# Performance work log

Measured on AMD Instinct MI355X. Metric: run time of the kernel, lower is better.

Reference implementation:

```python
import math
import jax
import jax.numpy as jnp
import numpy as np

B, T, D = 1, 2048, 1024
H, KV, DH = 16, 4, 64
E, TOPK, DFF = 32, 4, 1024
WINDOW = 128
EPS = 1e-5
ROPE_BASE = 150000.0
ROPE_SCALE = 32.0


def setup_inputs() -> dict:
    key = jax.random.key(0)
    ks = jax.random.split(key, 12)
    s = 0.02  # init scale for stability
    return {
        "x": jax.random.normal(ks[0], (B, T, D), jnp.float32),
        "attn_norm_w": 1.0 + 0.02 * jax.random.normal(ks[1], (D,), jnp.float32),
        "ffn_norm_w": 1.0 + 0.02 * jax.random.normal(ks[2], (D,), jnp.float32),
        "qkv_w": s * jax.random.normal(ks[3], (D, H * DH + 2 * KV * DH), jnp.float32),
        "qkv_b": s * jax.random.normal(ks[4], (H * DH + 2 * KV * DH,), jnp.float32),
        "proj_w": s * jax.random.normal(ks[5], (H * DH, D), jnp.float32),
        "proj_b": s * jax.random.normal(ks[6], (D,), jnp.float32),
        "attn_sink": 0.5 * jax.random.normal(ks[7], (H,), jnp.float32),
        "gate_w": s * jax.random.normal(ks[8], (D, E), jnp.float32),
        "gate_b": s * jax.random.normal(ks[9], (E,), jnp.float32),
        "W_up": s * jax.random.normal(ks[10], (E, D, 2 * DFF), jnp.float32),
        "W_down": s * jax.random.normal(ks[11], (E, DFF, D), jnp.float32),
    }


def _rmsnorm(x, w):
    rms = jax.lax.rsqrt(jnp.mean(x * x, axis=-1, keepdims=True) + EPS)
    return w * (x * rms)


def _apply_rope(x, sin, cos):
    # x: [B, h, T, dh]; sin/cos: [T, dh//2] -> interleaved rotation
    x1, x2 = x[..., ::2], x[..., 1::2]
    out = jnp.stack([x1 * cos - x2 * sin, x1 * sin + x2 * cos], axis=-1)
    return out.reshape(x.shape)


def reference(x, attn_norm_w, ffn_norm_w, qkv_w, qkv_b, proj_w, proj_b,
              attn_sink, gate_w, gate_b, W_up, W_down):
    Bx, Tx, Dx = x.shape
    # ---- attention branch ----
    h = _rmsnorm(x, attn_norm_w)
    qkv = h @ qkv_w + qkv_b
    q = qkv[..., : H * DH].reshape(Bx, Tx, H, DH).transpose(0, 2, 1, 3)
    k = qkv[..., H * DH : H * DH + KV * DH].reshape(Bx, Tx, KV, DH).transpose(0, 2, 1, 3)
    v = qkv[..., H * DH + KV * DH :].reshape(Bx, Tx, KV, DH).transpose(0, 2, 1, 3)
    # RoPE angles: pos/scale * base^{-2i/dh}
    pos = jnp.arange(Tx, dtype=jnp.float32) / ROPE_SCALE
    inv_freq = 1.0 / (ROPE_BASE ** (jnp.arange(0, DH, 2, dtype=jnp.float32) / DH))
    freqs = pos[:, None] * inv_freq[None, :]  # [T, DH//2]
    sin, cos = jnp.sin(freqs), jnp.cos(freqs)
    q = _apply_rope(q, sin, cos)
    k = _apply_rope(k, sin, cos)
    rep = H // KV
    k = jnp.repeat(k, rep, axis=1)
    v = jnp.repeat(v, rep, axis=1)
    logits = jnp.einsum('bhqd,bhkd->bhqk', q, k) / math.sqrt(DH)
    i = jnp.arange(Tx)[:, None]
    j = jnp.arange(Tx)[None, :]
    mask = (j > i) | (i - j > WINDOW)  # sliding-window causal
    logits = jnp.where(mask, -jnp.inf, logits)
    lse = jax.nn.logsumexp(logits, axis=-1, keepdims=True)  # [B,H,T,1]
    denom_log = jnp.logaddexp(lse, attn_sink.reshape(1, H, 1, 1))
    attn = jnp.exp(logits - denom_log)  # rows sum to < 1 due to sink
    y = jnp.einsum('bhqk,bhkd->bhqd', attn, v)
    y = y.transpose(0, 2, 1, 3).reshape(Bx, Tx, H * DH)
    x = x + (y @ proj_w + proj_b)
    # ---- token-choice MoE branch ----
    h2 = _rmsnorm(x, ffn_norm_w).reshape(Bx * Tx, Dx)
    glogits = h2 @ gate_w + gate_b  # [N, E]
    topv, topi = jax.lax.top_k(glogits, TOPK)
    gw = jax.nn.softmax(topv, axis=-1)  # [N, TOPK]
    N = Bx * Tx
    combine = jnp.zeros((N, E), x.dtype).at[jnp.arange(N)[:, None], topi].add(gw)
    def body(acc, we):
        wu, wd, ce = we  # [D,2DFF], [DFF,D], [N]
        ug = h2 @ wu
        u, g = ug[:, :DFF], ug[:, DFF:]
        return acc + ce[:, None] * ((jax.nn.silu(g) * u) @ wd), None
    y2, _ = jax.lax.scan(body, jnp.zeros_like(h2), (W_up, W_down, combine.T))
    return x + y2.reshape(Bx, Tx, Dx)
```

## Files before the change

### kernel.cpp

```cpp
#include <hip/hip_runtime.h>
#include <hip/hip_bf16.h>

#define NEx 32
#define QKVN 1536
#define MAXTILES 96

typedef __attribute__((ext_vector_type(4))) float f32x4_t;
typedef __attribute__((ext_vector_type(8))) __bf16 bf16x8_t;

__device__ __forceinline__ unsigned short f2bfu(float f) {
  union { float f; unsigned int u; } a; a.f = f;
  unsigned int r = a.u + 0x7fffu + ((a.u >> 16) & 1u);
  return (unsigned short)(r >> 16);
}
__device__ __forceinline__ float bf2f(unsigned short u) {
  union { unsigned int u; float f; } a; a.u = ((unsigned int)u) << 16; return a.f;
}
__device__ __forceinline__ uint2 pack4u(unsigned short a, unsigned short b,
                                        unsigned short c, unsigned short d) {
  return make_uint2((unsigned int)a | ((unsigned int)b << 16),
                    (unsigned int)c | ((unsigned int)d << 16));
}
__device__ __forceinline__ void split2(float v, unsigned short& hi, unsigned short& lo) {
  hi = f2bfu(v);
  lo = f2bfu(v - bf2f(hi));
}
typedef const __attribute__((address_space(1))) void* gas_t;
typedef __attribute__((address_space(3))) void* las_t;
__device__ __forceinline__ void gl16(const void* g, void* l) {
  __builtin_amdgcn_global_load_lds((gas_t)g, (las_t)l, 16, 0, 0);
}

template<int SPLIT>
__global__ __launch_bounds__(256) void k_wT(const float* __restrict__ in,
    unsigned short* __restrict__ outh, unsigned short* __restrict__ outl, int N) {
  __shared__ float T[64][68];
  int k0 = blockIdx.x * 64, n0 = blockIdx.y * 64, e = blockIdx.z;
  const float* src = in + (size_t)e * 1024 * N;
  int t = threadIdx.x;
  int rk = t >> 2, c4 = (t & 3) * 4;
#pragma unroll
  for (int j = 0; j < 4; ++j) {
    int col = c4 + j * 16;
    f32x4_t v = *(const f32x4_t*)(src + (size_t)(k0 + rk) * N + n0 + col);
    *(f32x4_t*)&T[rk][col] = v;
  }
  __syncthreads();
  int nn = t >> 2, kc0 = (t & 3) * 16;
  size_t orow = ((size_t)e * N + n0 + nn) * 1024 + k0;
#pragma unroll
  for (int j = 0; j < 2; ++j) {
    int kc = kc0 + j * 8;
    unsigned short hi[8], lo[8];
#pragma unroll
    for (int q = 0; q < 8; ++q) split2(T[kc + q][nn], hi[q], lo[q]);
    uint2 a = pack4u(hi[0], hi[1], hi[2], hi[3]);
    uint2 b = pack4u(hi[4], hi[5], hi[6], hi[7]);
    *(uint4*)(outh + orow + kc) = make_uint4(a.x, a.y, b.x, b.y);
    if (SPLIT) {
      uint2 c = pack4u(lo[0], lo[1], lo[2], lo[3]);
      uint2 d = pack4u(lo[4], lo[5], lo[6], lo[7]);
      *(uint4*)(outl + orow + kc) = make_uint4(c.x, c.y, d.x, d.y);
    }
  }
}

__global__ __launch_bounds__(256) void k_rmsnorm_s(const float* __restrict__ x,
    const float* __restrict__ w, unsigned short* __restrict__ ph, unsigned short* __restrict__ pl) {
  int row = blockIdx.x, tid = threadIdx.x;
  f32x4_t v = *(const f32x4_t*)(x + (size_t)row * 1024 + tid * 4);
  float ss = v.x * v.x + v.y * v.y + v.z * v.z + v.w * v.w;
#pragma unroll
  for (int o = 32; o > 0; o >>= 1) ss += __shfl_xor(ss, o);
  __shared__ float red[4];
  if ((tid & 63) == 0) red[tid >> 6] = ss;
  __syncthreads();
  float sc = rsqrtf((red[0] + red[1] + red[2] + red[3]) * (1.f / 1024.f) + 1e-5f);
  const float* wr = w + tid * 4;
  ushort4 h4, l4;
  split2(v.x * sc * wr[0], h4.x, l4.x);
  split2(v.y * sc * wr[1], h4.y, l4.y);
  split2(v.z * sc * wr[2], h4.z, l4.z);
  split2(v.w * sc * wr[3], h4.w, l4.w);
  *(ushort4*)(ph + (size_t)row * 1024 + tid * 4) = h4;
  *(ushort4*)(pl + (size_t)row * 1024 + tid * 4) = l4;
}

__global__ __launch_bounds__(256) void k_rmsnorm_f(const float* __restrict__ x,
    const float* __restrict__ w, float* __restrict__ outf, unsigned short* __restrict__ outb,
    float* __restrict__ y2) {
  int row = blockIdx.x, tid = threadIdx.x;
  f32x4_t v = *(const f32x4_t*)(x + (size_t)row * 1024 + tid * 4);
  *(f32x4_t*)(y2 + (size_t)row * 1024 + tid * 4) = (f32x4_t){0.f, 0.f, 0.f, 0.f};
  float ss = v.x * v.x + v.y * v.y + v.z * v.z + v.w * v.w;
#pragma unroll
  for (int o = 32; o > 0; o >>= 1) ss += __shfl_xor(ss, o);
  __shared__ float red[4];
  if ((tid & 63) == 0) red[tid >> 6] = ss;
  __syncthreads();
  float sc = rsqrtf((red[0] + red[1] + red[2] + red[3]) * (1.f / 1024.f) + 1e-5f);
  const float* wr = w + tid * 4;
  f32x4_t o4;
  o4.x = v.x * sc * wr[0]; o4.y = v.y * sc * wr[1];
  o4.z = v.z * sc * wr[2]; o4.w = v.w * sc * wr[3];
  *(f32x4_t*)(outf + (size_t)row * 1024 + tid * 4) = o4;
  ushort4 b4;
  b4.x = f2bfu(o4.x); b4.y = f2bfu(o4.y); b4.z = f2bfu(o4.z); b4.w = f2bfu(o4.w);
  *(ushort4*)(outb + (size_t)row * 1024 + tid * 4) = b4;
}

template<int RES>
__global__ __launch_bounds__(256) void k_gemm_s(
    const unsigned short* __restrict__ Ahg, const unsigned short* __restrict__ Alg,
    const unsigned short* __restrict__ BhT, const unsigned short* __restrict__ BlT,
    const float* __restrict__ bias, const float* __restrict__ res,
    float* __restrict__ C, int N) {
  __shared__ unsigned short Ah[64 * 32], Al[64 * 32], Bh[128 * 32], Bl[128 * 32];
  int tid = threadIdx.x, lane = tid & 63, w = tid >> 6;
  int m0 = blockIdx.y * 64, n0 = blockIdx.x * 128;
  int wm = (w >> 1) * 32, wn = (w & 1) * 64;
  int rl = lane >> 2, koff = (lane & 3) * 8;
  const unsigned short* agh = Ahg + (size_t)(m0 + w * 16 + rl) * 1024 + koff;
  const unsigned short* agl = Alg + (size_t)(m0 + w * 16 + rl) * 1024 + koff;
  const unsigned short* bgh0 = BhT + (size_t)(n0 + (w * 2 + 0) * 16 + rl) * 1024 + koff;
  const unsigned short* bgh1 = BhT + (size_t)(n0 + (w * 2 + 1) * 16 + rl) * 1024 + koff;
  const unsigned short* bgl0 = BlT + (size_t)(n0 + (w * 2 + 0) * 16 + rl) * 1024 + koff;
  const unsigned short* bgl1 = BlT + (size_t)(n0 + (w * 2 + 1) * 16 + rl) * 1024 + koff;
  f32x4_t acc[2][4];
#pragma unroll
  for (int i = 0; i < 2; ++i)
#pragma unroll
    for (int j = 0; j < 4; ++j) acc[i][j] = (f32x4_t){0.f, 0.f, 0.f, 0.f};
  int fr = lane & 15, fc = (lane >> 4) * 8;
  for (int k0 = 0; k0 < 1024; k0 += 32) {
    gl16(agh + k0, (char*)Ah + w * 1024);
    gl16(agl + k0, (char*)Al + w * 1024);
    gl16(bgh0 + k0, (char*)Bh + (w * 2 + 0) * 1024);
    gl16(bgh1 + k0, (char*)Bh + (w * 2 + 1) * 1024);
    gl16(bgl0 + k0, (char*)Bl + (w * 2 + 0) * 1024);
    gl16(bgl1 + k0, (char*)Bl + (w * 2 + 1) * 1024);
    __syncthreads();
    bf16x8_t fah[2], fal[2], fbh[4], fbl[4];
#pragma unroll
    for (int mi = 0; mi < 2; ++mi) {
      fah[mi] = *(const bf16x8_t*)(Ah + (wm + mi * 16 + fr) * 32 + fc);
      fal[mi] = *(const bf16x8_t*)(Al + (wm + mi * 16 + fr) * 32 + fc);
    }
#pragma unroll
    for (int nj = 0; nj < 4; ++nj) {
      fbh[nj] = *(const bf16x8_t*)(Bh + (wn + nj * 16 + fr) * 32 + fc);
      fbl[nj] = *(const bf16x8_t*)(Bl + (wn + nj * 16 + fr) * 32 + fc);
    }
#pragma unroll
    for (int mi = 0; mi < 2; ++mi)
#pragma unroll
      for (int nj = 0; nj < 4; ++nj) {
        acc[mi][nj] = __builtin_amdgcn_mfma_f32_16x16x32_bf16(fah[mi], fbh[nj], acc[mi][nj], 0, 0, 0);
        acc[mi][nj] = __builtin_amdgcn_mfma_f32_16x16x32_bf16(fah[mi], fbl[nj], acc[mi][nj], 0, 0, 0);
        acc[mi][nj] = __builtin_amdgcn_mfma_f32_16x16x32_bf16(fal[mi], fbh[nj], acc[mi][nj], 0, 0, 0);
      }
    __syncthreads();
  }
  int frow = (lane >> 4) * 4;
#pragma unroll
  for (int mi = 0; mi < 2; ++mi)
#pragma unroll
    for (int nj = 0; nj < 4; ++nj) {
      int col = n0 + wn + nj * 16 + fr;
      float bv = bias[col];
#pragma unroll
      for (int r = 0; r < 4; ++r) {
        int row = m0 + wm + mi * 16 + frow + r;
        float v = acc[mi][nj][r] + bv;
        if (RES) v += res[(size_t)row * N + col];
        C[(size_t)row * N + col] = v;
      }
    }
}

__global__ __launch_bounds__(256) void k_rope(float* __restrict__ qkv) {
  int idx = blockIdx.x * 256 + threadIdx.x;
  int i = idx & 31;
  int r5 = idx >> 5;
  int hd = r5 % 20, t = r5 / 20;
  int col = (hd < 16) ? hd * 64 : 1024 + (hd - 16) * 64;
  float* p = qkv + (size_t)t * QKVN + col + 2 * i;
  float2 v = *(float2*)p;
  float invf = exp2f(-(float)i * (17.194602975157967f / 32.f));
  float ang = ((float)t * (1.f / 32.f)) * invf;
  float s, c;
  sincosf(ang, &s, &c);
  float2 o; o.x = v.x * c - v.y * s; o.y = v.x * s + v.y * c;
  *(float2*)p = o;
}

__global__ __launch_bounds__(256) void k_attn(const float* __restrict__ qkv,
    const float* __restrict__ sink, unsigned short* __restrict__ yh,
    unsigned short* __restrict__ yl) {
  __shared__ float Kl[72 * 65];
  __shared__ float Vl[72 * 64];
  __shared__ float ql[16][64];
  __shared__ float pl[4][128];
  int i0 = blockIdx.x * 16, hh = blockIdx.y;
  int g = hh >> 2;
  int jb = i0 - 128; if (jb < 0) jb = 0;
  int nk = i0 + 16 - jb;
  int tid = threadIdx.x, wid = tid >> 6, lane = tid & 63;
  {
    int r = tid >> 4, d4 = (tid & 15) * 4;
    *(f32x4_t*)&ql[r][d4] = *(const f32x4_t*)(qkv + (size_t)(i0 + r) * QKVN + hh * 64 + d4);
  }
  float sk = sink[hh];
  float m_[4], s_[4], y_[4];
#pragma unroll
  for (int qq = 0; qq < 4; ++qq) { m_[qq] = sk; s_[qq] = 0.f; y_[qq] = 0.f; }
  int nch = (nk + 71) / 72;
  int cbase = 0;
  for (int ch = 0; ch < nch; ++ch) {
    int csz = nk - cbase; if (csz > 72) csz = 72;
    __syncthreads();
    for (int id = tid; id < csz * 16; id += 256) {
      int c = id >> 4, d4 = (id & 15) * 4;
      const float* kp = qkv + (size_t)(jb + cbase + c) * QKVN + 1024 + g * 64 + d4;
      *(f32x4_t*)&Kl[c * 65 + d4] = *(const f32x4_t*)kp;
      *(f32x4_t*)&Vl[c * 64 + d4] = *(const f32x4_t*)(kp + 256);
    }
    __syncthreads();
#pragma unroll
    for (int qq = 0; qq < 4; ++qq) {
      int qr = wid * 4 + qq;
      int cm = i0 + qr - jb;
      int s1 = lane + 64;
      int r1 = (s1 < csz) ? s1 : (csz - 1);
      const float* k0p = Kl + lane * 65;
      const float* k1p = Kl + r1 * 65;
      float a0 = 0.f, a1 = 0.f;
#pragma unroll 4
      for (int d = 0; d < 64; ++d) {
        float qd = ql[qr][d];
        a0 += qd * k0p[d];
        a1 += qd * k1p[d];
      }
      int c0 = cbase + lane, c1 = cbase + s1;
      bool ok0 = (lane < csz) && (c0 <= cm) && (c0 >= cm - 128);
      bool ok1 = (s1 < csz) && (c1 <= cm) && (c1 >= cm - 128);
      float l0 = ok0 ? a0 * 0.125f : -1e30f;
      float l1 = ok1 ? a1 * 0.125f : -1e30f;
      float mc = fmaxf(l0, l1);
#pragma unroll
      for (int o = 32; o > 0; o >>= 1) mc = fmaxf(mc, __shfl_xor(mc, o));
      float mo = m_[qq];
      float mn = fmaxf(mo, mc);
      float fac = __expf(mo - mn);
      float p0 = __expf(l0 - mn), p1 = __expf(l1 - mn);
      float ps = p0 + p1;
#pragma unroll
      for (int o = 32; o > 0; o >>= 1) ps += __shfl_xor(ps, o);
      m_[qq] = mn;
      s_[qq] = s_[qq] * fac + ps;
      pl[wid][lane] = p0;
      pl[wid][s1] = p1;
      __syncthreads();
      float y = y_[qq] * fac;
      for (int s = 0; s < csz; ++s) y += pl[wid][s] * Vl[s * 64 + lane];
      y_[qq] = y;
      __syncthreads();
    }
    cbase += csz;
  }
#pragma unroll
  for (int qq = 0; qq < 4; ++qq) {
    float inv = 1.f / (s_[qq] + __expf(sk - m_[qq]));
    int i = i0 + wid * 4 + qq;
    unsigned short hi, lo;
    split2(y_[qq] * inv, hi, lo);
    yh[(size_t)i * 1024 + hh * 64 + lane] = hi;
    yl[(size_t)i * 1024 + hh * 64 + lane] = lo;
  }
}

__global__ __launch_bounds__(64) void k_gate(const float* __restrict__ h2f,
    const float* __restrict__ gw, const float* __restrict__ gb,
    int* __restrict__ texp, float* __restrict__ twt) {
  int t = blockIdx.x, l = threadIdx.x;
  int e = l & 31, half = l >> 5;
  const float* hr = h2f + (size_t)t * 1024 + half * 512;
  const float* wp = gw + (size_t)half * 512 * 32 + e;
  float s = 0;
  for (int d = 0; d < 512; ++d) s += hr[d] * wp[(size_t)d * 32];
  s += __shfl_xor(s, 32);
  __shared__ float gl[32];
  if (l < 32) gl[l] = s + gb[e];
  __syncthreads();
  if (l == 0) {
    int bi[4]; float bv[4];
    for (int j = 0; j < 4; ++j) {
      int mi_ = 0; float mv = gl[0];
      for (int q = 1; q < 32; ++q) if (gl[q] > mv) { mv = gl[q]; mi_ = q; }
      bi[j] = mi_; bv[j] = mv; gl[mi_] = -1e30f;
    }
    float mx = bv[0], sum = 0, wv[4];
    for (int j = 0; j < 4; ++j) { wv[j] = __expf(bv[j] - mx); sum += wv[j]; }
    float inv = 1.f / sum;
    for (int j = 0; j < 4; ++j) { texp[t * 4 + j] = bi[j]; twt[t * 4 + j] = wv[j] * inv; }
  }
}

__global__ __launch_bounds__(256) void k_moe_count(const int* __restrict__ texp, int* __restrict__ cnt) {
  int e = blockIdx.x, tid = threadIdx.x;
  int c = 0;
  for (int i = tid; i < 8192; i += 256) c += (texp[i] == e);
#pragma unroll
  for (int o = 32; o > 0; o >>= 1) c += __shfl_xor(c, o);
  __shared__ int red[4];
  if ((tid & 63) == 0) red[tid >> 6] = c;
  __syncthreads();
  if (tid == 0) cnt[e] = red[0] + red[1] + red[2] + red[3];
}

__global__ void k_moe_off(const int* __restrict__ cnt, int* __restrict__ off,
                          int* __restrict__ tiles) {
  if (threadIdx.x == 0) {
    int s = 0, t = 0;
    for (int e = 0; e < NEx; ++e) {
      off[e] = s;
      int nt = (cnt[e] + 127) >> 7;
      for (int j = 0; j < nt; ++j) tiles[t++] = e | (j << 8);
      s += cnt[e];
    }
    for (; t < MAXTILES; ++t) tiles[t] = -1;
  }
}

__global__ __launch_bounds__(256) void k_moe_assign(const int* __restrict__ texp,
    const float* __restrict__ twt, const int* __restrict__ off,
    int* __restrict__ slot_token, float* __restrict__ slot_wt) {
  int e = blockIdx.x, tid = threadIdx.x;
  int b0 = tid * 32;
  int c = 0;
  for (int i = 0; i < 32; ++i) c += (texp[b0 + i] == e);
  __shared__ int pre[256];
  pre[tid] = c;
  __syncthreads();
  for (int d = 1; d < 256; d <<= 1) {
    int v = (tid >= d) ? pre[tid - d] : 0;
    __syncthreads();
    pre[tid] += v;
    __syncthreads();
  }
  int run = off[e] + pre[tid] - c;
  for (int i = 0; i < 32; ++i) {
    int idx = b0 + i;
    if (texp[idx] == e) {
      slot_token[run] = idx >> 2;
      slot_wt[run] = twt[idx];
      ++run;
    }
  }
}

__global__ __launch_bounds__(256) void k_moe_up(const unsigned short* __restrict__ h2b,
    const unsigned short* __restrict__ WupT, const int* __restrict__ cnt,
    const int* __restrict__ off, const int* __restrict__ tiles,
    const int* __restrict__ slot_token, unsigned short* __restrict__ act) {
  int code = tiles[blockIdx.y];
  if (code < 0) return;
  int e = code & 255;
  int m0 = (code >> 8) << 7;
  int ne = cnt[e];
  int n0 = blockIdx.x * 64;
  int base = off[e];
  __shared__ unsigned short Asm[128 * 32];
  __shared__ unsigned short Bsm[128 * 32];
  int tid = threadIdx.x, lane = tid & 63, w = tid >> 6;
  int rl = lane >> 2, koff = (lane & 3) * 8;
  const unsigned short* ag[2];
  const unsigned short* bg[2];
#pragma unroll
  for (int i = 0; i < 2; ++i) {
    int row = (w * 2 + i) * 16 + rl;
    int tok = (m0 + row < ne) ? slot_token[base + m0 + row] : 0;
    ag[i] = h2b + (size_t)tok * 1024 + koff;
    int grow = (row < 64) ? (n0 + row) : (1024 + n0 + row - 64);
    bg[i] = WupT + (size_t)e * 2048 * 1024 + (size_t)grow * 1024 + koff;
  }
  f32x4_t acc[2][8];
#pragma unroll
  for (int i = 0; i < 2; ++i)
#pragma unroll
    for (int j = 0; j < 8; ++j) acc[i][j] = (f32x4_t){0.f, 0.f, 0.f, 0.f};
  int fr = lane & 15, fc = (lane >> 4) * 8;
  for (int k0 = 0; k0 < 1024; k0 += 32) {
    gl16(ag[0] + k0, (char*)Asm + (w * 2 + 0) * 1024);
    gl16(ag[1] + k0, (char*)Asm + (w * 2 + 1) * 1024);
    gl16(bg[0] + k0, (char*)Bsm + (w * 2 + 0) * 1024);
    gl16(bg[1] + k0, (char*)Bsm + (w * 2 + 1) * 1024);
    __syncthreads();
    bf16x8_t af[2], bfr[8];
#pragma unroll
    for (int mi = 0; mi < 2; ++mi)
      af[mi] = *(const bf16x8_t*)(Asm + (w * 32 + mi * 16 + fr) * 32 + fc);
#pragma unroll
    for (int nj = 0; nj < 8; ++nj)
      bfr[nj] = *(const bf16x8_t*)(Bsm + (nj * 16 + fr) * 32 + fc);
#pragma unroll
    for (int mi = 0; mi < 2; ++mi)
#pragma unroll
      for (int nj = 0; nj < 8; ++nj)
        acc[mi][nj] = __builtin_amdgcn_mfma_f32_16x16x32_bf16(af[mi], bfr[nj], acc[mi][nj], 0, 0, 0);
    __syncthreads();
  }
  int frow = (lane >> 4) * 4;
#pragma unroll
  for (int mi = 0; mi < 2; ++mi)
#pragma unroll
    for (int r = 0; r < 4; ++r) {
      int row = m0 + w * 32 + mi * 16 + frow + r;
      if (row < ne) {
#pragma unroll
        for (int nj = 0; nj < 4; ++nj) {
          float u = acc[mi][nj][r];
          float gg = acc[mi][nj + 4][r];
          float sig = 1.f / (1.f + __expf(-gg));
          act[(size_t)(base + row) * 1024 + n0 + nj * 16 + fr] = f2bfu(u * gg * sig);
        }
      }
    }
}

__global__ __launch_bounds__(256) void k_moe_down(const unsigned short* __restrict__ act,
    const unsigned short* __restrict__ WdnT, const int* __restrict__ cnt,
    const int* __restrict__ off, const int* __restrict__ tiles,
    const int* __restrict__ slot_token, const float* __restrict__ slot_wt,
    float* __restrict__ y2) {
  int code = tiles[blockIdx.y];
  if (code < 0) return;
  int e = code & 255;
  int m0 = (code >> 8) << 7;
  int ne = cnt[e];
  int n0 = blockIdx.x * 128;
  int base = off[e];
  __shared__ unsigned short Asm[128 * 32];
  __shared__ unsigned short Bsm[128 * 32];
  int tid = threadIdx.x, lane = tid & 63, w = tid >> 6;
  int wm = (w >> 1) * 64, wn = (w & 1) * 64;
  int rl = lane >> 2, koff = (lane & 3) * 8;
  const unsigned short* ag[2];
  const unsigned short* bg[2];
#pragma unroll
  for (int i = 0; i < 2; ++i) {
    int row = (w * 2 + i) * 16 + rl;
    ag[i] = act + (size_t)(base + m0 + row) * 1024 + koff;
    bg[i] = WdnT + (size_t)e * 1024 * 1024 + (size_t)(n0 + row) * 1024 + koff;
  }
  f32x4_t acc[4][4];
#pragma unroll
  for (int i = 0; i < 4; ++i)
#pragma unroll
    for (int j = 0; j < 4; ++j) acc[i][j] = (f32x4_t){0.f, 0.f, 0.f, 0.f};
  int fr = lane & 15, fc = (lane >> 4) * 8;
  for (int k0 = 0; k0 < 1024; k0 += 32) {
    gl16(ag[0] + k0, (char*)Asm + (w * 2 + 0) * 1024);
    gl16(ag[1] + k0, (char*)Asm + (w * 2 + 1) * 1024);
    gl16(bg[0] + k0, (char*)Bsm + (w * 2 + 0) * 1024);
    gl16(bg[1] + k0, (char*)Bsm + (w * 2 + 1) * 1024);
    __syncthreads();
    bf16x8_t af[4], bfr[4];
#pragma unroll
    for (int mi = 0; mi < 4; ++mi)
      af[mi] = *(const bf16x8_t*)(Asm + (wm + mi * 16 + fr) * 32 + fc);
#pragma unroll
    for (int nj = 0; nj < 4; ++nj)
      bfr[nj] = *(const bf16x8_t*)(Bsm + (wn + nj * 16 + fr) * 32 + fc);
#pragma unroll
    for (int mi = 0; mi < 4; ++mi)
#pragma unroll
      for (int nj = 0; nj < 4; ++nj)
        acc[mi][nj] = __builtin_amdgcn_mfma_f32_16x16x32_bf16(af[mi], bfr[nj], acc[mi][nj], 0, 0, 0);
    __syncthreads();
  }
  int frow = (lane >> 4) * 4;
#pragma unroll
  for (int mi = 0; mi < 4; ++mi)
#pragma unroll
    for (int r = 0; r < 4; ++r) {
      int row = m0 + wm + mi * 16 + frow + r;
      if (row < ne) {
        int slot = base + row;
        int token = slot_token[slot];
        float wt = slot_wt[slot];
#pragma unroll
        for (int nj = 0; nj < 4; ++nj) {
          int col = n0 + wn + nj * 16 + fr;
          atomicAdd(&y2[(size_t)token * 1024 + col], wt * acc[mi][nj][r]);
        }
      }
    }
}

__global__ __launch_bounds__(256) void k_final(const float* __restrict__ x1,
    const float* __restrict__ y2, float* __restrict__ out) {
  int idx = blockIdx.x * 256 + threadIdx.x;
  f32x4_t a = *(const f32x4_t*)(x1 + (size_t)idx * 4);
  f32x4_t b = *(const f32x4_t*)(y2 + (size_t)idx * 4);
  a = a + b;
  *(f32x4_t*)(out + (size_t)idx * 4) = a;
}

extern "C" void kernel_launch(void* const* d_in, const int* in_sizes, int n_in,
                              void* d_out, int out_size, void* d_ws, size_t ws_size,
                              hipStream_t stream) {
  const float* x           = (const float*)d_in[0];
  const float* attn_norm_w = (const float*)d_in[1];
  const float* ffn_norm_w  = (const float*)d_in[2];
  const float* qkv_w       = (const float*)d_in[3];
  const float* qkv_b       = (const float*)d_in[4];
  const float* proj_w      = (const float*)d_in[5];
  const float* proj_b      = (const float*)d_in[6];
  const float* attn_sink   = (const float*)d_in[7];
  const float* gate_w      = (const float*)d_in[8];
  const float* gate_b      = (const float*)d_in[9];
  const float* W_up        = (const float*)d_in[10];
  const float* W_down      = (const float*)d_in[11];
  float* out = (float*)d_out;

  char* ws = (char*)d_ws;
  size_t o = 0;
  auto alloc = [&](size_t bytes) -> void* {
    void* p = ws + o;
    o = (o + bytes + 255) & ~(size_t)255;
    return p;
  };
  unsigned short* WT      = (unsigned short*)alloc((size_t)32 * 2048 * 1024 * 2);
  unsigned short* qkvThi  = (unsigned short*)alloc((size_t)1536 * 1024 * 2);
  unsigned short* qkvTlo  = (unsigned short*)alloc((size_t)1536 * 1024 * 2);
  unsigned short* projThi = (unsigned short*)alloc((size_t)1024 * 1024 * 2);
  unsigned short* projTlo = (unsigned short*)alloc((size_t)1024 * 1024 * 2);
  unsigned short* pAhi    = (unsigned short*)alloc((size_t)2048 * 1024 * 2);
  unsigned short* pAlo    = (unsigned short*)alloc((size_t)2048 * 1024 * 2);
  float* qkv              = (float*)alloc((size_t)2048 * 1536 * 4);
  float* x1               = (float*)alloc((size_t)2048 * 1024 * 4);
  unsigned short* act     = (unsigned short*)alloc((size_t)(8192 + 128) * 1024 * 2);
  float* y2               = (float*)alloc((size_t)2048 * 1024 * 4);
  int* texp               = (int*)alloc(8192 * 4);
  float* twt              = (float*)alloc(8192 * 4);
  int* cnt                = (int*)alloc(256);
  int* offs               = (int*)alloc(256);
  int* tiles              = (int*)alloc(MAXTILES * 4);
  int* slot_token         = (int*)alloc(8192 * 4);
  float* slot_wt          = (float*)alloc(8192 * 4);
  float* h2f              = qkv;
  unsigned short* h2b     = (unsigned short*)(qkv + (size_t)2048 * 1024);

  k_wT<1><<<dim3(16, 24, 1), 256, 0, stream>>>(qkv_w, qkvThi, qkvTlo, 1536);
  k_wT<1><<<dim3(16, 16, 1), 256, 0, stream>>>(proj_w, projThi, projTlo, 1024);
  k_wT<0><<<dim3(16, 32, 32), 256, 0, stream>>>(W_up, WT, nullptr, 2048);

  k_rmsnorm_s<<<2048, 256, 0, stream>>>(x, attn_norm_w, pAhi, pAlo);
  k_gemm_s<0><<<dim3(12, 32), 256, 0, stream>>>(pAhi, pAlo, qkvThi, qkvTlo, qkv_b, nullptr, qkv, 1536);
  k_rope<<<5120, 256, 0, stream>>>(qkv);
  k_attn<<<dim3(128, 16), 256, 0, stream>>>(qkv, attn_sink, pAhi, pAlo);
  k_gemm_s<1><<<dim3(8, 32), 256, 0, stream>>>(pAhi, pAlo, projThi, projTlo, proj_b, x, x1, 1024);
  k_rmsnorm_f<<<2048, 256, 0, stream>>>(x1, ffn_norm_w, h2f, h2b, y2);
  k_gate<<<2048, 64, 0, stream>>>(h2f, gate_w, gate_b, texp, twt);
  k_moe_count<<<32, 256, 0, stream>>>(texp, cnt);
  k_moe_off<<<1, 64, 0, stream>>>(cnt, offs, tiles);
  k_moe_assign<<<32, 256, 0, stream>>>(texp, twt, offs, slot_token, slot_wt);
  k_moe_up<<<dim3(16, MAXTILES), 256, 0, stream>>>(h2b, WT, cnt, offs, tiles, slot_token, act);
  k_wT<0><<<dim3(16, 16, 32), 256, 0, stream>>>(W_down, WT, nullptr, 1024);
  k_moe_down<<<dim3(8, MAXTILES), 256, 0, stream>>>(act, WT, cnt, offs, tiles, slot_token, slot_wt, y2);
  k_final<<<2048, 256, 0, stream>>>(x1, y2, out);
}
```

Before: 475.9 us.

## Fuse gate into FFN RMSNorm and double-buffer LDS in GEMM kernels

The router gate matmul and top-k selection now run inside the FFN RMSNorm kernel, so the fp32 normalized activations no longer go to global memory and no separate gate launch is needed. All three MFMA GEMM kernels (split-precision projection, MoE up, MoE down) now use two LDS buffers and prefetch the next K tile while the current one is computed. The per-iteration barrier count drops from two to one. The cost is double the shared memory, which may lower occupancy, and 32 accumulator registers plus a long shuffle reduction per thread in the fused norm kernel.

```diff
diff --git a/kernel.cpp b/kernel.cpp
--- a/kernel.cpp
+++ b/kernel.cpp
@@ -86,9 +86,10 @@
   *(ushort4*)(pl + (size_t)row * 1024 + tid * 4) = l4;
 }
 
-__global__ __launch_bounds__(256) void k_rmsnorm_f(const float* __restrict__ x,
-    const float* __restrict__ w, float* __restrict__ outf, unsigned short* __restrict__ outb,
-    float* __restrict__ y2) {
+__global__ __launch_bounds__(256) void k_rmsnorm_g(const float* __restrict__ x,
+    const float* __restrict__ w, const float* __restrict__ gw, const float* __restrict__ gb,
+    unsigned short* __restrict__ outb, float* __restrict__ y2,
+    int* __restrict__ texp, float* __restrict__ twt) {
   int row = blockIdx.x, tid = threadIdx.x;
   f32x4_t v = *(const f32x4_t*)(x + (size_t)row * 1024 + tid * 4);
   *(f32x4_t*)(y2 + (size_t)row * 1024 + tid * 4) = (f32x4_t){0.f, 0.f, 0.f, 0.f};
@@ -100,13 +101,55 @@
   __syncthreads();
   float sc = rsqrtf((red[0] + red[1] + red[2] + red[3]) * (1.f / 1024.f) + 1e-5f);
   const float* wr = w + tid * 4;
-  f32x4_t o4;
-  o4.x = v.x * sc * wr[0]; o4.y = v.y * sc * wr[1];
-  o4.z = v.z * sc * wr[2]; o4.w = v.w * sc * wr[3];
-  *(f32x4_t*)(outf + (size_t)row * 1024 + tid * 4) = o4;
+  float h[4];
+  h[0] = v.x * sc * wr[0]; h[1] = v.y * sc * wr[1];
+  h[2] = v.z * sc * wr[2]; h[3] = v.w * sc * wr[3];
   ushort4 b4;
-  b4.x = f2bfu(o4.x); b4.y = f2bfu(o4.y); b4.z = f2bfu(o4.z); b4.w = f2bfu(o4.w);
+  b4.x = f2bfu(h[0]); b4.y = f2bfu(h[1]); b4.z = f2bfu(h[2]); b4.w = f2bfu(h[3]);
   *(ushort4*)(outb + (size_t)row * 1024 + tid * 4) = b4;
+  float p[32];
+#pragma unroll
+  for (int e = 0; e < 32; ++e) p[e] = 0.f;
+#pragma unroll
+  for (int j = 0; j < 4; ++j) {
+    float hj = h[j];
+    const float* gr = gw + (size_t)(4 * tid + j) * 32;
+#pragma unroll
+    for (int e4 = 0; e4 < 8; ++e4) {
+      f32x4_t g4 = *(const f32x4_t*)(gr + e4 * 4);
+      p[e4 * 4 + 0] += hj * g4.x;
+      p[e4 * 4 + 1] += hj * g4.y;
+      p[e4 * 4 + 2] += hj * g4.z;
+      p[e4 * 4 + 3] += hj * g4.w;
+    }
+  }
+#pragma unroll
+  for (int o = 32; o > 0; o >>= 1) {
+#pragma unroll
+    for (int e = 0; e < 32; ++e) p[e] += __shfl_xor(p[e], o);
+  }
+  __shared__ float gl[4][32];
+  if ((tid & 63) == 0) {
+    int w4 = tid >> 6;
+#pragma unroll
+    for (int e = 0; e < 32; ++e) gl[w4][e] = p[e];
+  }
+  __syncthreads();
+  if (tid == 0) {
+    float g[32];
+#pragma unroll
+    for (int e = 0; e < 32; ++e) g[e] = gl[0][e] + gl[1][e] + gl[2][e] + gl[3][e] + gb[e];
+    int bi[4]; float bv[4];
+    for (int j = 0; j < 4; ++j) {
+      int mi_ = 0; float mv = g[0];
+      for (int q = 1; q < 32; ++q) if (g[q] > mv) { mv = g[q]; mi_ = q; }
+      bi[j] = mi_; bv[j] = mv; g[mi_] = -1e30f;
+    }
+    float mx = bv[0], sum = 0, wv[4];
+    for (int j = 0; j < 4; ++j) { wv[j] = __expf(bv[j] - mx); sum += wv[j]; }
+    float inv = 1.f / sum;
+    for (int j = 0; j < 4; ++j) { texp[row * 4 + j] = bi[j]; twt[row * 4 + j] = wv[j] * inv; }
+  }
 }
 
 template<int RES>
@@ -115,7 +158,8 @@
     const unsigned short* __restrict__ BhT, const unsigned short* __restrict__ BlT,
     const float* __restrict__ bias, const float* __restrict__ res,
     float* __restrict__ C, int N) {
-  __shared__ unsigned short Ah[64 * 32], Al[64 * 32], Bh[128 * 32], Bl[128 * 32];
+  __shared__ unsigned short Ah[2 * 64 * 32], Al[2 * 64 * 32];
+  __shared__ unsigned short Bh[2 * 128 * 32], Bl[2 * 128 * 32];
   int tid = threadIdx.x, lane = tid & 63, w = tid >> 6;
   int m0 = blockIdx.y * 64, n0 = blockIdx.x * 128;
   int wm = (w >> 1) * 32, wn = (w & 1) * 64;
@@ -126,30 +170,39 @@
   const unsigned short* bgh1 = BhT + (size_t)(n0 + (w * 2 + 1) * 16 + rl) * 1024 + koff;
   const unsigned short* bgl0 = BlT + (size_t)(n0 + (w * 2 + 0) * 16 + rl) * 1024 + koff;
   const unsigned short* bgl1 = BlT + (size_t)(n0 + (w * 2 + 1) * 16 + rl) * 1024 + koff;
+  auto STAGE = [&](int b, int k0) {
+    gl16(agh + k0, (char*)(Ah + b * 2048) + w * 1024);
+    gl16(agl + k0, (char*)(Al + b * 2048) + w * 1024);
+    gl16(bgh0 + k0, (char*)(Bh + b * 4096) + (w * 2 + 0) * 1024);
+    gl16(bgh1 + k0, (char*)(Bh + b * 4096) + (w * 2 + 1) * 1024);
+    gl16(bgl0 + k0, (char*)(Bl + b * 4096) + (w * 2 + 0) * 1024);
+    gl16(bgl1 + k0, (char*)(Bl + b * 4096) + (w * 2 + 1) * 1024);
+  };
   f32x4_t acc[2][4];
 #pragma unroll
   for (int i = 0; i < 2; ++i)
 #pragma unroll
     for (int j = 0; j < 4; ++j) acc[i][j] = (f32x4_t){0.f, 0.f, 0.f, 0.f};
   int fr = lane & 15, fc = (lane >> 4) * 8;
+  STAGE(0, 0);
+  __syncthreads();
+  int cur = 0;
   for (int k0 = 0; k0 < 1024; k0 += 32) {
-    gl16(agh + k0, (char*)Ah + w * 1024);
-    gl16(agl + k0, (char*)Al + w * 1024);
-    gl16(bgh0 + k0, (char*)Bh + (w * 2 + 0) * 1024);
-    gl16(bgh1 + k0, (char*)Bh + (w * 2 + 1) * 1024);
-    gl16(bgl0 + k0, (char*)Bl + (w * 2 + 0) * 1024);
-    gl16(bgl1 + k0, (char*)Bl + (w * 2 + 1) * 1024);
-    __syncthreads();
+    if (k0 + 32 < 1024) STAGE(cur ^ 1, k0 + 32);
+    const unsigned short* Ahc = Ah + cur * 2048;
+    const unsigned short* Alc = Al + cur * 2048;
+    const unsigned short* Bhc = Bh + cur * 4096;
+    const unsigned short* Blc = Bl + cur * 4096;
     bf16x8_t fah[2], fal[2], fbh[4], fbl[4];
 #pragma unroll
     for (int mi = 0; mi < 2; ++mi) {
-      fah[mi] = *(const bf16x8_t*)(Ah + (wm + mi * 16 + fr) * 32 + fc);
-      fal[mi] = *(const bf16x8_t*)(Al + (wm + mi * 16 + fr) * 32 + fc);
+      fah[mi] = *(const bf16x8_t*)(Ahc + (wm + mi * 16 + fr) * 32 + fc);
+      fal[mi] = *(const bf16x8_t*)(Alc + (wm + mi * 16 + fr) * 32 + fc);
     }
 #pragma unroll
     for (int nj = 0; nj < 4; ++nj) {
-      fbh[nj] = *(const bf16x8_t*)(Bh + (wn + nj * 16 + fr) * 32 + fc);
-      fbl[nj] = *(const bf16x8_t*)(Bl + (wn + nj * 16 + fr) * 32 + fc);
+      fbh[nj] = *(const bf16x8_t*)(Bhc + (wn + nj * 16 + fr) * 32 + fc);
+      fbl[nj] = *(const bf16x8_t*)(Blc + (wn + nj * 16 + fr) * 32 + fc);
     }
 #pragma unroll
     for (int mi = 0; mi < 2; ++mi)
@@ -160,6 +213,7 @@
         acc[mi][nj] = __builtin_amdgcn_mfma_f32_16x16x32_bf16(fal[mi], fbh[nj], acc[mi][nj], 0, 0, 0);
       }
     __syncthreads();
+    cur ^= 1;
   }
   int frow = (lane >> 4) * 4;
 #pragma unroll
@@ -279,33 +333,6 @@
   }
 }
 
-__global__ __launch_bounds__(64) void k_gate(const float* __restrict__ h2f,
-    const float* __restrict__ gw, const float* __restrict__ gb,
-    int* __restrict__ texp, float* __restrict__ twt) {
-  int t = blockIdx.x, l = threadIdx.x;
-  int e = l & 31, half = l >> 5;
-  const float* hr = h2f + (size_t)t * 1024 + half * 512;
-  const float* wp = gw + (size_t)half * 512 * 32 + e;
-  float s = 0;
-  for (int d = 0; d < 512; ++d) s += hr[d] * wp[(size_t)d * 32];
-  s += __shfl_xor(s, 32);
-  __shared__ float gl[32];
-  if (l < 32) gl[l] = s + gb[e];
-  __syncthreads();
-  if (l == 0) {
-    int bi[4]; float bv[4];
-    for (int j = 0; j < 4; ++j) {
-      int mi_ = 0; float mv = gl[0];
-      for (int q = 1; q < 32; ++q) if (gl[q] > mv) { mv = gl[q]; mi_ = q; }
-      bi[j] = mi_; bv[j] = mv; gl[mi_] = -1e30f;
-    }
-    float mx = bv[0], sum = 0, wv[4];
-    for (int j = 0; j < 4; ++j) { wv[j] = __expf(bv[j] - mx); sum += wv[j]; }
-    float inv = 1.f / sum;
-    for (int j = 0; j < 4; ++j) { texp[t * 4 + j] = bi[j]; twt[t * 4 + j] = wv[j] * inv; }
-  }
-}
-
 __global__ __launch_bounds__(256) void k_moe_count(const int* __restrict__ texp, int* __restrict__ cnt) {
   int e = blockIdx.x, tid = threadIdx.x;
   int c = 0;
@@ -370,8 +397,8 @@
   int ne = cnt[e];
   int n0 = blockIdx.x * 64;
   int base = off[e];
-  __shared__ unsigned short Asm[128 * 32];
-  __shared__ unsigned short Bsm[128 * 32];
+  __shared__ unsigned short Asm[2 * 128 * 32];
+  __shared__ unsigned short Bsm[2 * 128 * 32];
   int tid = threadIdx.x, lane = tid & 63, w = tid >> 6;
   int rl = lane >> 2, koff = (lane & 3) * 8;
   const unsigned short* ag[2];
@@ -384,31 +411,39 @@
     int grow = (row < 64) ? (n0 + row) : (1024 + n0 + row - 64);
     bg[i] = WupT + (size_t)e * 2048 * 1024 + (size_t)grow * 1024 + koff;
   }
+  auto STAGE = [&](int b, int k0) {
+    gl16(ag[0] + k0, (char*)(Asm + b * 4096) + (w * 2 + 0) * 1024);
+    gl16(ag[1] + k0, (char*)(Asm + b * 4096) + (w * 2 + 1) * 1024);
+    gl16(bg[0] + k0, (char*)(Bsm + b * 4096) + (w * 2 + 0) * 1024);
+    gl16(bg[1] + k0, (char*)(Bsm + b * 4096) + (w * 2 + 1) * 1024);
+  };
   f32x4_t acc[2][8];
 #pragma unroll
   for (int i = 0; i < 2; ++i)
 #pragma unroll
     for (int j = 0; j < 8; ++j) acc[i][j] = (f32x4_t){0.f, 0.f, 0.f, 0.f};
   int fr = lane & 15, fc = (lane >> 4) * 8;
+  STAGE(0, 0);
+  __syncthreads();
+  int cur = 0;
   for (int k0 = 0; k0 < 1024; k0 += 32) {
-    gl16(ag[0] + k0, (char*)Asm + (w * 2 + 0) * 1024);
-    gl16(ag[1] + k0, (char*)Asm + (w * 2 + 1) * 1024);
-    gl16(bg[0] + k0, (char*)Bsm + (w * 2 + 0) * 1024);
-    gl16(bg[1] + k0, (char*)Bsm + (w * 2 + 1) * 1024);
-    __syncthreads();
+    if (k0 + 32 < 1024) STAGE(cur ^ 1, k0 + 32);
+    const unsigned short* Ac = Asm + cur * 4096;
+    const unsigned short* Bc = Bsm + cur * 4096;
     bf16x8_t af[2], bfr[8];
 #pragma unroll
     for (int mi = 0; mi < 2; ++mi)
-      af[mi] = *(const bf16x8_t*)(Asm + (w * 32 + mi * 16 + fr) * 32 + fc);
+      af[mi] = *(const bf16x8_t*)(Ac + (w * 32 + mi * 16 + fr) * 32 + fc);
 #pragma unroll
     for (int nj = 0; nj < 8; ++nj)
-      bfr[nj] = *(const bf16x8_t*)(Bsm + (nj * 16 + fr) * 32 + fc);
+      bfr[nj] = *(const bf16x8_t*)(Bc + (nj * 16 + fr) * 32 + fc);
 #pragma unroll
     for (int mi = 0; mi < 2; ++mi)
 #pragma unroll
       for (int nj = 0; nj < 8; ++nj)
         acc[mi][nj] = __builtin_amdgcn_mfma_f32_16x16x32_bf16(af[mi], bfr[nj], acc[mi][nj], 0, 0, 0);
     __syncthreads();
+    cur ^= 1;
   }
   int frow = (lane >> 4) * 4;
 #pragma unroll
@@ -440,8 +475,8 @@
   int ne = cnt[e];
   int n0 = blockIdx.x * 128;
   int base = off[e];
-  __shared__ unsigned short Asm[128 * 32];
-  __shared__ unsigned short Bsm[128 * 32];
+  __shared__ unsigned short Asm[2 * 128 * 32];
+  __shared__ unsigned short Bsm[2 * 128 * 32];
   int tid = threadIdx.x, lane = tid & 63, w = tid >> 6;
   int wm = (w >> 1) * 64, wn = (w & 1) * 64;
   int rl = lane >> 2, koff = (lane & 3) * 8;
@@ -453,31 +488,39 @@
     ag[i] = act + (size_t)(base + m0 + row) * 1024 + koff;
     bg[i] = WdnT + (size_t)e * 1024 * 1024 + (size_t)(n0 + row) * 1024 + koff;
   }
+  auto STAGE = [&](int b, int k0) {
+    gl16(ag[0] + k0, (char*)(Asm + b * 4096) + (w * 2 + 0) * 1024);
+    gl16(ag[1] + k0, (char*)(Asm + b * 4096) + (w * 2 + 1) * 1024);
+    gl16(bg[0] + k0, (char*)(Bsm + b * 4096) + (w * 2 + 0) * 1024);
+    gl16(bg[1] + k0, (char*)(Bsm + b * 4096) + (w * 2 + 1) * 1024);
+  };
   f32x4_t acc[4][4];
 #pragma unroll
   for (int i = 0; i < 4; ++i)
 #pragma unroll
     for (int j = 0; j < 4; ++j) acc[i][j] = (f32x4_t){0.f, 0.f, 0.f, 0.f};
   int fr = lane & 15, fc = (lane >> 4) * 8;
+  STAGE(0, 0);
+  __syncthreads();
+  int cur = 0;
   for (int k0 = 0; k0 < 1024; k0 += 32) {
-    gl16(ag[0] + k0, (char*)Asm + (w * 2 + 0) * 1024);
-    gl16(ag[1] + k0, (char*)Asm + (w * 2 + 1) * 1024);
-    gl16(bg[0] + k0, (char*)Bsm + (w * 2 + 0) * 1024);
-    gl16(bg[1] + k0, (char*)Bsm + (w * 2 + 1) * 1024);
-    __syncthreads();
+    if (k0 + 32 < 1024) STAGE(cur ^ 1, k0 + 32);
+    const unsigned short* Ac = Asm + cur * 4096;
+    const unsigned short* Bc = Bsm + cur * 4096;
     bf16x8_t af[4], bfr[4];
 #pragma unroll
     for (int mi = 0; mi < 4; ++mi)
-      af[mi] = *(const bf16x8_t*)(Asm + (wm + mi * 16 + fr) * 32 + fc);
+      af[mi] = *(const bf16x8_t*)(Ac + (wm + mi * 16 + fr) * 32 + fc);
 #pragma unroll
     for (int nj = 0; nj < 4; ++nj)
-      bfr[nj] = *(const bf16x8_t*)(Bsm + (wn + nj * 16 + fr) * 32 + fc);
+      bfr[nj] = *(const bf16x8_t*)(Bc + (wn + nj * 16 + fr) * 32 + fc);
 #pragma unroll
     for (int mi = 0; mi < 4; ++mi)
 #pragma unroll
       for (int nj = 0; nj < 4; ++nj)
         acc[mi][nj] = __builtin_amdgcn_mfma_f32_16x16x32_bf16(af[mi], bfr[nj], acc[mi][nj], 0, 0, 0);
     __syncthreads();
+    cur ^= 1;
   }
   int frow = (lane >> 4) * 4;
 #pragma unroll
@@ -549,8 +592,7 @@
   int* tiles              = (int*)alloc(MAXTILES * 4);
   int* slot_token         = (int*)alloc(8192 * 4);
   float* slot_wt          = (float*)alloc(8192 * 4);
-  float* h2f              = qkv;
-  unsigned short* h2b     = (unsigned short*)(qkv + (size_t)2048 * 1024);
+  unsigned short* h2b     = (unsigned short*)qkv;
 
   k_wT<1><<<dim3(16, 24, 1), 256, 0, stream>>>(qkv_w, qkvThi, qkvTlo, 1536);
   k_wT<1><<<dim3(16, 16, 1), 256, 0, stream>>>(proj_w, projThi, projTlo, 1024);
@@ -561,8 +603,7 @@
   k_rope<<<5120, 256, 0, stream>>>(qkv);
   k_attn<<<dim3(128, 16), 256, 0, stream>>>(qkv, attn_sink, pAhi, pAlo);
   k_gemm_s<1><<<dim3(8, 32), 256, 0, stream>>>(pAhi, pAlo, projThi, projTlo, proj_b, x, x1, 1024);
-  k_rmsnorm_f<<<2048, 256, 0, stream>>>(x1, ffn_norm_w, h2f, h2b, y2);
-  k_gate<<<2048, 64, 0, stream>>>(h2f, gate_w, gate_b, texp, twt);
+  k_rmsnorm_g<<<2048, 256, 0, stream>>>(x1, ffn_norm_w, gate_w, gate_b, h2b, y2, texp, twt);
   k_moe_count<<<32, 256, 0, stream>>>(texp, cnt);
   k_moe_off<<<1, 64, 0, stream>>>(cnt, offs, tiles);
   k_moe_assign<<<32, 256, 0, stream>>>(texp, twt, offs, slot_token, slot_wt);
```

Result: slower. 506.4 us (+6.4%).
